# Kernel tuning notes

Hardware: AMD Instinct MI355X
Metric: run time of the kernel (lower is better)

Reference implementation:

```python
import jax, jax.numpy as jnp
import numpy as np

N_NODES = 50000
N_EDGES = 800000
EPS = 1e-5
NEG_SLOPE = 0.2


def _gatv2(x, src, dst, Wl, bl, Wr, br, att, bias, concat, N):
    # PyG GATv2Conv: xl = lin_l(x) (source side), xr = lin_r(x) (target side)
    H, C = att.shape
    xl = (x @ Wl + bl).reshape(N, H, C)
    xr = (x @ Wr + br).reshape(N, H, C)
    # per-edge message: leaky_relu(xl[j] + xr[i]), attention logit = <att, .>
    z = xl[src] + xr[dst]                      # [E, H, C]
    z = jnp.where(z > 0, z, NEG_SLOPE * z)
    logits = jnp.einsum('ehc,hc->eh', z, att)  # [E, H]
    # segment softmax over incoming edges of each target node
    m = jax.lax.stop_gradient(jax.ops.segment_max(logits, dst, num_segments=N))
    p = jnp.exp(logits - m[dst])
    s = jax.ops.segment_sum(p, dst, num_segments=N)
    alpha = p / s[dst]                         # [E, H]
    out = jax.ops.segment_sum(xl[src] * alpha[..., None], dst, num_segments=N)  # [N, H, C]
    out = out.reshape(N, H * C) if concat else out.mean(axis=1)
    return out + bias


def _bn(x, g, b):
    mu = x.mean(axis=0)
    v = x.var(axis=0)
    return (x - mu) * jax.lax.rsqrt(v + EPS) * g + b


def setup_inputs() -> dict:
    key = jax.random.key(0)
    ks = jax.random.split(key, 16)
    x = jax.random.normal(ks[0], (N_NODES, 2), jnp.float32)
    edge_index = jax.random.randint(ks[1], (2, N_EDGES), 0, N_NODES, dtype=jnp.int64)

    def lin(k, i, o):
        return jax.random.normal(k, (i, o), jnp.float32) * (1.0 / np.sqrt(i))

    inp = {'x': x, 'edge_index': edge_index}
    # layer 1: in=2, heads=8, out=16, concat
    inp['W1l'] = lin(ks[2], 2, 128); inp['b1l'] = jnp.zeros((128,), jnp.float32)
    inp['W1r'] = lin(ks[3], 2, 128); inp['b1r'] = jnp.zeros((128,), jnp.float32)
    inp['a1'] = jax.random.normal(ks[4], (8, 16), jnp.float32) * 0.1
    inp['bias1'] = jnp.zeros((128,), jnp.float32)
    inp['g1'] = jnp.ones((128,), jnp.float32); inp['be1'] = jnp.zeros((128,), jnp.float32)
    # layer 2: in=128, heads=4, out=16, concat
    inp['W2l'] = lin(ks[5], 128, 64); inp['b2l'] = jnp.zeros((64,), jnp.float32)
    inp['W2r'] = lin(ks[6], 128, 64); inp['b2r'] = jnp.zeros((64,), jnp.float32)
    inp['a2'] = jax.random.normal(ks[7], (4, 16), jnp.float32) * 0.1
    inp['bias2'] = jnp.zeros((64,), jnp.float32)
    inp['g2'] = jnp.ones((64,), jnp.float32); inp['be2'] = jnp.zeros((64,), jnp.float32)
    # layer 3: in=64, heads=1, out=2, mean (concat=False)
    inp['W3l'] = lin(ks[8], 64, 2); inp['b3l'] = jnp.zeros((2,), jnp.float32)
    inp['W3r'] = lin(ks[9], 64, 2); inp['b3r'] = jnp.zeros((2,), jnp.float32)
    inp['a3'] = jax.random.normal(ks[10], (1, 2), jnp.float32) * 0.1
    inp['bias3'] = jnp.zeros((2,), jnp.float32)
    return inp


def reference(x, edge_index, W1l, b1l, W1r, b1r, a1, bias1, g1, be1,
              W2l, b2l, W2r, b2r, a2, bias2, g2, be2,
              W3l, b3l, W3r, b3r, a3, bias3):
    N = x.shape[0]
    loops = jnp.arange(N, dtype=edge_index.dtype)
    src = jnp.concatenate([edge_index[0], loops])  # add self loops (PyG default)
    dst = jnp.concatenate([edge_index[1], loops])
    h = _gatv2(x, src, dst, W1l, b1l, W1r, b1r, a1, bias1, True, N)
    h = jax.nn.elu(_bn(h, g1, be1))  # dropout is identity in eval
    h = _gatv2(h, src, dst, W2l, b2l, W2r, b2r, a2, bias2, True, N)
    h = jax.nn.elu(_bn(h, g2, be2))
    return _gatv2(h, src, dst, W3l, b3l, W3r, b3r, a3, bias3, False, N)
```

## Files before the change

kernel.cpp:

```cpp
#include <hip/hip_runtime.h>
#include <hip/hip_bf16.h>

#define N_NODES 50000
#define N_E0    800000
#define N_ET    850000
#define EPSBN   1e-5f
#define LOG2E   1.4426950408889634f

#define LEAKY(z) fmaxf((z), 0.2f * (z))

#define OFF_C 0
#define OFF_A (128*N_NODES)
#define OFF_B (192*N_NODES)
#define OFF_STATS (256*N_NODES)
#define OFF_S1R (OFF_STATS + 512)
#define OFF_S2R (OFF_S1R + 16384)
#define OFF_P (OFF_S2R + 8192)
#define N_PARAM_TOT 118312
#define OFF_ROWPTR (OFF_P + N_PARAM_TOT)
#define OFF_DEG    (OFF_ROWPTR + 50001)
#define OFF_CURSOR (OFF_DEG + 50000)
#define OFF_BSUM   (OFF_CURSOR + 50000)
#define OFF_COL    (OFF_BSUM + 256)
#define OFF_FLAGS  (OFF_COL + 850064)
#define OFF_SCNT   (OFF_FLAGS + 2)

#define BK_CAP 131072
#define BK_CHUNK 2048

typedef float v2f __attribute__((ext_vector_type(2)));

__device__ __forceinline__ v2f ld2(const float* p) { return *(const v2f*)p; }
__device__ __forceinline__ v2f fma2(v2f a, v2f b, v2f c) {
    return __builtin_elementwise_fma(a, b, c);
}
__device__ __forceinline__ v2f max2(v2f a, v2f b) {
    return __builtin_elementwise_max(a, b);
}

__device__ __forceinline__ float bf2f(unsigned short u) {
    return __uint_as_float(((unsigned int)u) << 16);
}
__device__ __forceinline__ unsigned short f2bf(float f) {
    unsigned int u = __float_as_uint(f);
    u += 0x7FFFu + ((u >> 16) & 1u);
    return (unsigned short)(u >> 16);
}

__global__ void prep_kernel(const unsigned short* xr, const int* ei, int* flags,
                            int* deg, float* stats, float* s1r, float* s2r, int* scnt,
                            int* col) {
    int i = blockIdx.x * 256 + threadIdx.x;
    if (i < N_NODES) deg[i] = 0;
    if (i < 512) stats[i] = 0.f;
    if (i < 16384) s1r[i] = 0.f;
    if (i < 8192)  s2r[i] = 0.f;
    if (i < 8) scnt[i] = 0;
    if (i < 64) col[N_ET + i] = 0;
    if (blockIdx.x == 0) {
        __shared__ int c1, c2;
        if (threadIdx.x == 0) { c1 = 0; c2 = 0; }
        __syncthreads();
        int t = threadIdx.x;
        int l1 = 0, l2 = 0;
        for (int k = t; k < 2048; k += 256) {
            float v = bf2f(xr[k]);
            if (!(fabsf(v) <= 100.0f)) l1++;
            if (ei[2 * k + 1] != 0) l2++;
        }
        atomicAdd(&c1, l1);
        atomicAdd(&c2, l2);
        __syncthreads();
        if (t == 0) {
            flags[0] = (c1 > 16) ? 1 : 0;
            flags[1] = (c2 == 0) ? 1 : 0;
        }
    }
}

struct ParamPtrs { const void* p[23]; };

__global__ void convert_kernel(ParamPtrs ps, float* dst, const int* flags) {
    const int sizes[23] = {100000, 256,128,256,128,128,128,128,128,
                           8192,64,8192,64,64,64,64,64,
                           128,2,128,2,2,2};
    int g = blockIdx.x * 256 + threadIdx.x;
    if (g >= N_PARAM_TOT) return;
    int t = 0, off = g;
    while (off >= sizes[t]) { off -= sizes[t]; t++; }
    float v;
    if (flags[0]) v = ((const float*)ps.p[t])[off];
    else          v = bf2f(((const unsigned short*)ps.p[t])[off]);
    if (t == 5 || t == 13 || t == 21) v *= LOG2E;
    dst[g] = v;
}

__global__ void bucket_kernel(const int* ei, const int* flags, int* scnt,
                              int* dstb, int* srcb, int* deg) {
    __shared__ int lcnt[8];
    __shared__ int lbase[8];
    int tid = threadIdx.x;
    if (tid < 8) lcnt[tid] = 0;
    __syncthreads();
    int base_e = blockIdx.x * BK_CHUNK;
    int i64 = flags[1];
    int src[8], dst[8], pos[8];
    #pragma unroll
    for (int u = 0; u < 8; u++) {
        int e = base_e + u * 256 + tid;
        if (e < N_ET) {
            int s, d;
            if (e < N_E0) {
                d = i64 ? ei[2 * (N_E0 + e)] : ei[N_E0 + e];
                s = i64 ? ei[2 * e] : ei[e];
            } else { s = d = e - N_E0; }
            src[u] = s; dst[u] = d;
            pos[u] = atomicAdd(&lcnt[d / 6250], 1);
            atomicAdd(&deg[d], 1);
        } else dst[u] = -1;
    }
    __syncthreads();
    if (tid < 8) lbase[tid] = atomicAdd(&scnt[tid], lcnt[tid]);
    __syncthreads();
    #pragma unroll
    for (int u = 0; u < 8; u++) {
        if (dst[u] >= 0) {
            int st = dst[u] / 6250;
            int gp = st * BK_CAP + lbase[st] + pos[u];
            dstb[gp] = dst[u];
            srcb[gp] = src[u];
        }
    }
}

__global__ void scan1_kernel(const int* deg, int* row_ptr, int* bsum) {
    __shared__ int sh[256];
    int i = blockIdx.x * 256 + threadIdx.x;
    int v = (i < N_NODES) ? deg[i] : 0;
    sh[threadIdx.x] = v;
    __syncthreads();
    for (int off = 1; off < 256; off <<= 1) {
        int t = (threadIdx.x >= off) ? sh[threadIdx.x - off] : 0;
        __syncthreads();
        sh[threadIdx.x] += t;
        __syncthreads();
    }
    if (i < N_NODES) row_ptr[i] = sh[threadIdx.x] - v;
    if (threadIdx.x == 255) bsum[blockIdx.x] = sh[255];
}

__global__ void scan23_kernel(int* row_ptr, int* cursor, const int* bsum) {
    __shared__ int sh[256];
    int t = threadIdx.x;
    int v = (t < 196) ? bsum[t] : 0;
    sh[t] = v;
    __syncthreads();
    for (int off = 1; off < 256; off <<= 1) {
        int u = (t >= off) ? sh[t - off] : 0;
        __syncthreads();
        sh[t] += u;
        __syncthreads();
    }
    int prefix = (blockIdx.x == 0) ? 0 : sh[blockIdx.x - 1];
    int i = blockIdx.x * 256 + t;
    if (i < N_NODES) {
        int r = row_ptr[i] + prefix;
        row_ptr[i] = r;
        cursor[i] = r;
    }
    if (i == 0) row_ptr[N_NODES] = N_ET;
}

__global__ void scatter2_kernel(const int* scnt, const int* dstb, const int* srcb,
                                int* cursor, int* col) {
    int stripe = blockIdx.x & 7;
    int bi = blockIdx.x >> 3;
    int cnt = scnt[stripe];
    int off = stripe * BK_CAP;
    for (int t = bi * 256 + threadIdx.x; t < cnt; t += 32 * 256) {
        int d = dstb[off + t];
        int pos = atomicAdd(&cursor[d], 1);
        col[pos] = srcb[off + t];
    }
}

__global__ void __launch_bounds__(256) gather1_kernel(
    const int* row_ptr, const int* col, const float* x,
    const float* W1l, const float* b1l, const float* W1r, const float* b1r,
    const float* att, const float* bias, unsigned int* Cb, float* s1r)
{
    int gid = blockIdx.x * 256 + threadIdx.x;
    int n = gid >> 6;
    int lane = threadIdx.x & 63;
    int eslot = lane >> 4;
    int slot  = lane & 15;
    int c0 = slot << 3;

    int base = __builtin_amdgcn_readfirstlane(row_ptr[n]);
    int deg  = __builtin_amdgcn_readfirstlane(row_ptr[n + 1]) - base;

    v2f w0[4], w1[4], at[4], K[4];
    v2f xd = ld2(x + 2 * n);
    v2f xdx = {xd.x, xd.x}, xdy = {xd.y, xd.y};
    #pragma unroll
    for (int k = 0; k < 4; k++) {
        w0[k] = ld2(W1l + c0 + 2 * k);
        w1[k] = ld2(W1l + 128 + c0 + 2 * k);
        at[k] = ld2(att + c0 + 2 * k);
        v2f wr0 = ld2(W1r + c0 + 2 * k);
        v2f wr1 = ld2(W1r + 128 + c0 + 2 * k);
        v2f bb  = ld2(b1r + c0 + 2 * k) + ld2(b1l + c0 + 2 * k);
        K[k] = fma2(xdx, wr0, fma2(xdy, wr1, bb));
    }

    float S0 = 0.f, S1 = 0.f, SP = 0.f;
    for (int j0 = 0; j0 < deg; j0 += 64) {
        int cnt = deg - j0; if (cnt > 64) cnt = 64;
        int msrc = col[base + j0 + lane];
        v2f xsv = ld2(x + 2 * msrc);
        for (int jb = 0; jb < cnt; jb += 4) {
            int e = jb + eslot;
            float x0s = __shfl(xsv.x, e, 64);
            float x1s = __shfl(xsv.y, e, 64);
            v2f x0 = {x0s, x0s}, x1 = {x1s, x1s};
            v2f lg = {0.f, 0.f};
            #pragma unroll
            for (int k = 0; k < 4; k++) {
                v2f t = fma2(x1, w1[k], fma2(x0, w0[k], K[k]));
                lg = fma2(max2(t, 0.2f * t), at[k], lg);
            }
            float logit = lg.x + lg.y;
            logit += __shfl_xor(logit, 1, 64);
            float p = (e < cnt) ? exp2f(logit) : 0.f;
            S0 = fmaf(p, x0s, S0);
            S1 = fmaf(p, x1s, S1);
            SP += p;
        }
    }
    #pragma unroll
    for (int m = 16; m <= 32; m <<= 1) {
        S0 += __shfl_xor(S0, m, 64);
        S1 += __shfl_xor(S1, m, 64);
        SP += __shfl_xor(SP, m, 64);
    }
    float inv = 1.f / SP;
    float t0 = S0 * inv, t1 = S1 * inv;

    int hsrc = (lane >> 3) << 1;
    float t0o = __shfl(t0, hsrc, 64);
    float t1o = __shfl(t1, hsrc, 64);
    v2f w0o = ld2(W1l + 2 * lane);
    v2f w1o = ld2(W1l + 128 + 2 * lane);
    v2f bo  = ld2(b1l + 2 * lane) + ld2(bias + 2 * lane);
    float ox = fmaf(w0o.x, t0o, fmaf(w1o.x, t1o, bo.x));
    float oy = fmaf(w0o.y, t0o, fmaf(w1o.y, t1o, bo.y));
    Cb[n * 64 + lane] = ((unsigned int)f2bf(oy) << 16) | f2bf(ox);

    __shared__ float sred[4][128];
    __shared__ float qred[4][128];
    int wv = threadIdx.x >> 6;
    sred[wv][2 * lane]     = ox;
    sred[wv][2 * lane + 1] = oy;
    qred[wv][2 * lane]     = ox * ox;
    qred[wv][2 * lane + 1] = oy * oy;
    __syncthreads();
    int t = threadIdx.x;
    float a;
    if (t < 128) a = sred[0][t] + sred[1][t] + sred[2][t] + sred[3][t];
    else { int c = t - 128; a = qred[0][c] + qred[1][c] + qred[2][c] + qred[3][c]; }
    atomicAdd(&s1r[(blockIdx.x & 63) * 256 + t], a);
}

__global__ void red1_kernel(const float* s1r, const float* g1, const float* be1,
                            float* stats) {
    __shared__ float ls[256];
    int t = threadIdx.x;
    float a = 0.f;
    for (int r = 0; r < 64; r++) a += s1r[r * 256 + t];
    ls[t] = a;
    __syncthreads();
    if (t < 128) {
        float mu = ls[t] * (1.0f / N_NODES);
        float var = ls[128 + t] * (1.0f / N_NODES) - mu * mu;
        float sc = g1[t] * rsqrtf(var + EPSBN);
        stats[t] = sc;
        stats[128 + t] = be1[t] - mu * sc;
    }
}

__global__ void __launch_bounds__(256) lin2_kernel(
    const unsigned int* Cb, const float* stats, const float* Wl, const float* bl,
    const float* Wr, const float* br, unsigned short* xl2b, float* xr2)
{
    __shared__ float h[64 * 132];
    int tid = threadIdx.x;
    int nb = blockIdx.x * 64;
    for (int i = tid; i < 64 * 64; i += 256) {
        int ni = i >> 6, kp = i & 63;
        int n = nb + ni;
        int k = 2 * kp;
        float v0 = 0.f, v1 = 0.f;
        if (n < N_NODES) {
            unsigned int pk = Cb[n * 64 + kp];
            float b0 = fmaf(__uint_as_float(pk << 16),        stats[k],     stats[128 + k]);
            float b1 = fmaf(__uint_as_float(pk & 0xffff0000u), stats[k + 1], stats[128 + k + 1]);
            v0 = b0 > 0.f ? b0 : __expf(b0) - 1.f;
            v1 = b1 > 0.f ? b1 : __expf(b1) - 1.f;
        }
        h[ni * 132 + k]     = v0;
        h[ni * 132 + k + 1] = v1;
    }
    __syncthreads();
    int kt = (tid & 15) * 4;
    int nt = (tid >> 4) * 4;
    float accl[4][4], accr[4][4];
    #pragma unroll
    for (int i = 0; i < 4; i++) {
        #pragma unroll
        for (int k = 0; k < 4; k++) { accl[i][k] = 0.f; accr[i][k] = 0.f; }
    }
    for (int j = 0; j < 128; j += 4) {
        float4 hv[4];
        #pragma unroll
        for (int i = 0; i < 4; i++)
            hv[i] = *(const float4*)&h[(nt + i) * 132 + j];
        #pragma unroll
        for (int jj = 0; jj < 4; jj++) {
            float4 wl4 = *(const float4*)&Wl[(j + jj) * 64 + kt];
            float4 wr4 = *(const float4*)&Wr[(j + jj) * 64 + kt];
            #pragma unroll
            for (int i = 0; i < 4; i++) {
                float hvv = (jj == 0) ? hv[i].x : (jj == 1) ? hv[i].y :
                            (jj == 2) ? hv[i].z : hv[i].w;
                accl[i][0] += hvv * wl4.x; accl[i][1] += hvv * wl4.y;
                accl[i][2] += hvv * wl4.z; accl[i][3] += hvv * wl4.w;
                accr[i][0] += hvv * wr4.x; accr[i][1] += hvv * wr4.y;
                accr[i][2] += hvv * wr4.z; accr[i][3] += hvv * wr4.w;
            }
        }
    }
    float4 blv = *(const float4*)&bl[kt];
    float4 brv = *(const float4*)&br[kt];
    #pragma unroll
    for (int i = 0; i < 4; i++) {
        int n = nb + nt + i;
        if (n < N_NODES) {
            ushort4 ob;
            ob.x = f2bf(accl[i][0] + blv.x);
            ob.y = f2bf(accl[i][1] + blv.y);
            ob.z = f2bf(accl[i][2] + blv.z);
            ob.w = f2bf(accl[i][3] + blv.w);
            *(ushort4*)&xl2b[n * 64 + kt] = ob;
            float4 o;
            o.x = accr[i][0] + brv.x; o.y = accr[i][1] + brv.y;
            o.z = accr[i][2] + brv.z; o.w = accr[i][3] + brv.w;
            *(float4*)&xr2[n * 64 + kt] = o;
        }
    }
}

__global__ void __launch_bounds__(256) gather2_kernel(
    const int* row_ptr, const int* col, const unsigned short* xl2b, const float* xr2,
    const float* att, const float* bias, float* C, float* s2r)
{
    int gid = blockIdx.x * 256 + threadIdx.x;
    int n = gid >> 6;
    int lane = threadIdx.x & 63;
    int grp = lane >> 4;
    int cidx = lane & 15;
    float4 xrv = *(const float4*)(xr2 + n * 64 + 4 * cidx);
    float4 atv = *(const float4*)(att + 4 * cidx);
    int base = __builtin_amdgcn_readfirstlane(row_ptr[n]);
    int deg  = __builtin_amdgcn_readfirstlane(row_ptr[n + 1]) - base;
    float4 acc = make_float4(0.f, 0.f, 0.f, 0.f);
    float den = 0.f;
    for (int j0 = 0; j0 < deg; j0 += 64) {
        int cnt = deg - j0; if (cnt > 64) cnt = 64;
        int msrc = col[base + j0 + lane];
        for (int j4 = 0; j4 < cnt; j4 += 8) {
            int e0 = j4 + grp, e1 = j4 + 4 + grp;
            int s0 = __shfl(msrc, e0, 64);
            int s1 = __shfl(msrc, e1, 64);
            bool v0 = e0 < cnt, v1 = e1 < cnt;
            s0 = v0 ? s0 : 0;
            s1 = v1 ? s1 : 0;
            uint2 ba = *(const uint2*)(xl2b + (size_t)s0 * 64 + 4 * cidx);
            uint2 bb = *(const uint2*)(xl2b + (size_t)s1 * 64 + 4 * cidx);
            float a0 = __uint_as_float(ba.x << 16);
            float a1 = __uint_as_float(ba.x & 0xffff0000u);
            float a2 = __uint_as_float(ba.y << 16);
            float a3 = __uint_as_float(ba.y & 0xffff0000u);
            float b0 = __uint_as_float(bb.x << 16);
            float b1 = __uint_as_float(bb.x & 0xffff0000u);
            float b2 = __uint_as_float(bb.y << 16);
            float b3 = __uint_as_float(bb.y & 0xffff0000u);
            float pa = LEAKY(a0 + xrv.x) * atv.x;
            pa = fmaf(LEAKY(a1 + xrv.y), atv.y, pa);
            pa = fmaf(LEAKY(a2 + xrv.z), atv.z, pa);
            pa = fmaf(LEAKY(a3 + xrv.w), atv.w, pa);
            float pb = LEAKY(b0 + xrv.x) * atv.x;
            pb = fmaf(LEAKY(b1 + xrv.y), atv.y, pb);
            pb = fmaf(LEAKY(b2 + xrv.z), atv.z, pb);
            pb = fmaf(LEAKY(b3 + xrv.w), atv.w, pb);
            pa += __shfl_xor(pa, 1, 64);
            pa += __shfl_xor(pa, 2, 64);
            pb += __shfl_xor(pb, 1, 64);
            pb += __shfl_xor(pb, 2, 64);
            float ea = v0 ? exp2f(pa) : 0.f;
            float eb = v1 ? exp2f(pb) : 0.f;
            acc.x = fmaf(ea, a0, acc.x); acc.x = fmaf(eb, b0, acc.x);
            acc.y = fmaf(ea, a1, acc.y); acc.y = fmaf(eb, b1, acc.y);
            acc.z = fmaf(ea, a2, acc.z); acc.z = fmaf(eb, b2, acc.z);
            acc.w = fmaf(ea, a3, acc.w); acc.w = fmaf(eb, b3, acc.w);
            den += ea + eb;
        }
    }
    acc.x += __shfl_xor(acc.x, 16, 64); acc.x += __shfl_xor(acc.x, 32, 64);
    acc.y += __shfl_xor(acc.y, 16, 64); acc.y += __shfl_xor(acc.y, 32, 64);
    acc.z += __shfl_xor(acc.z, 16, 64); acc.z += __shfl_xor(acc.z, 32, 64);
    acc.w += __shfl_xor(acc.w, 16, 64); acc.w += __shfl_xor(acc.w, 32, 64);
    den += __shfl_xor(den, 16, 64);
    den += __shfl_xor(den, 32, 64);
    float inv = 1.f / den;
    float4 bi = *(const float4*)(bias + 4 * cidx);
    float4 o;
    o.x = fmaf(acc.x, inv, bi.x);
    o.y = fmaf(acc.y, inv, bi.y);
    o.z = fmaf(acc.z, inv, bi.z);
    o.w = fmaf(acc.w, inv, bi.w);
    if (lane < 16) *(float4*)(C + n * 64 + 4 * cidx) = o;
    __shared__ float sred[4][64];
    __shared__ float qred[4][64];
    int wv = threadIdx.x >> 6;
    if (lane < 16) {
        int c = 4 * cidx;
        sred[wv][c]     = o.x; qred[wv][c]     = o.x * o.x;
        sred[wv][c + 1] = o.y; qred[wv][c + 1] = o.y * o.y;
        sred[wv][c + 2] = o.z; qred[wv][c + 2] = o.z * o.z;
        sred[wv][c + 3] = o.w; qred[wv][c + 3] = o.w * o.w;
    }
    __syncthreads();
    int t = threadIdx.x;
    if (t < 128) {
        float a;
        if (t < 64) a = sred[0][t] + sred[1][t] + sred[2][t] + sred[3][t];
        else { int c = t - 64; a = qred[0][c] + qred[1][c] + qred[2][c] + qred[3][c]; }
        atomicAdd(&s2r[(blockIdx.x & 63) * 128 + t], a);
    }
}

__global__ void red2_kernel(const float* s2r, const float* g2, const float* be2,
                            float* stats) {
    __shared__ float ls[128];
    int t = threadIdx.x;
    float a = 0.f;
    for (int r = 0; r < 64; r++) a += s2r[r * 128 + t];
    ls[t] = a;
    __syncthreads();
    if (t < 64) {
        float mu = ls[t] * (1.0f / N_NODES);
        float var = ls[64 + t] * (1.0f / N_NODES) - mu * mu;
        float sc = g2[t] * rsqrtf(var + EPSBN);
        stats[t] = sc;
        stats[64 + t] = be2[t] - mu * sc;
    }
}

__global__ void __launch_bounds__(256) lin3_kernel(
    const float* C, const float* stats2,
    const float* Wl, const float* bl, const float* Wr, const float* br,
    float* xl3, float* xr3)
{
    int gid = blockIdx.x * 256 + threadIdx.x;
    int n = gid >> 6;
    int lane = threadIdx.x & 63;
    if (n >= N_NODES) return;
    float v = fmaf(C[n * 64 + lane], stats2[lane], stats2[64 + lane]);
    float h = v > 0.f ? v : __expf(v) - 1.f;
    float2 wlv = *(const float2*)(Wl + 2 * lane);
    float2 wrv = *(const float2*)(Wr + 2 * lane);
    float a0 = h * wlv.x, a1 = h * wlv.y;
    float r0 = h * wrv.x, r1 = h * wrv.y;
    #pragma unroll
    for (int m = 1; m < 64; m <<= 1) {
        a0 += __shfl_xor(a0, m, 64);
        a1 += __shfl_xor(a1, m, 64);
        r0 += __shfl_xor(r0, m, 64);
        r1 += __shfl_xor(r1, m, 64);
    }
    if (lane == 0) {
        xl3[2 * n]     = a0 + bl[0];
        xl3[2 * n + 1] = a1 + bl[1];
        xr3[2 * n]     = r0 + br[0];
        xr3[2 * n + 1] = r1 + br[1];
    }
}

__global__ void __launch_bounds__(256) gather3_kernel(
    const int* row_ptr, const int* col,
    const float* xl3, const float* xr3,
    const float* att, const float* bias,
    void* out, const int* flags) {
    int gid = blockIdx.x * 256 + threadIdx.x;
    int n = gid >> 2;
    int q = threadIdx.x & 3;
    if (n >= N_NODES) return;
    float a0 = att[0], a1 = att[1];
    float xr0 = xr3[2 * n], xr1 = xr3[2 * n + 1];
    float acc0 = 0.f, acc1 = 0.f, den = 0.f;
    int e0 = row_ptr[n], e1 = row_ptr[n + 1];
    for (int e = e0 + q; e < e1; e += 4) {
        int src = col[e];
        float2 xs = *(const float2*)(xl3 + 2 * src);
        float z0 = LEAKY(xs.x + xr0);
        float z1 = LEAKY(xs.y + xr1);
        float p = exp2f(fmaf(z0, a0, z1 * a1));
        acc0 = fmaf(p, xs.x, acc0);
        acc1 = fmaf(p, xs.y, acc1);
        den += p;
    }
    acc0 += __shfl_xor(acc0, 1, 64); acc0 += __shfl_xor(acc0, 2, 64);
    acc1 += __shfl_xor(acc1, 1, 64); acc1 += __shfl_xor(acc1, 2, 64);
    den  += __shfl_xor(den, 1, 64);  den  += __shfl_xor(den, 2, 64);
    if (q == 0) {
        float inv = 1.f / den;
        float v0 = fmaf(acc0, inv, bias[0]);
        float v1 = fmaf(acc1, inv, bias[1]);
        if (flags[0]) {
            ((float*)out)[2 * n] = v0;
            ((float*)out)[2 * n + 1] = v1;
        } else {
            ((__hip_bfloat16*)out)[2 * n] = __float2bfloat16(v0);
            ((__hip_bfloat16*)out)[2 * n + 1] = __float2bfloat16(v1);
        }
    }
}

extern "C" void kernel_launch(void* const* d_in, const int* in_sizes, int n_in,
                              void* d_out, int out_size, void* d_ws, size_t ws_size,
                              hipStream_t stream) {
    float* W = (float*)d_ws;
    float* C = W + OFF_C;
    float* A = W + OFF_A;
    float* B = W + OFF_B;
    float* STATS = W + OFF_STATS;
    float* S1R = W + OFF_S1R;
    float* S2R = W + OFF_S2R;
    float* P = W + OFF_P;
    int* ROWPTR = (int*)(W + OFF_ROWPTR);
    int* DEG    = (int*)(W + OFF_DEG);
    int* CURSOR = (int*)(W + OFF_CURSOR);
    int* BSUM   = (int*)(W + OFF_BSUM);
    int* COL    = (int*)(W + OFF_COL);
    int* FLAGS  = (int*)(W + OFF_FLAGS);
    int* SCNT   = (int*)(W + OFF_SCNT);
    int* DSTB   = (int*)(W + OFF_C);
    int* SRCB   = DSTB + 8 * BK_CAP;

    const int* ei = (const int*)d_in[1];

    float* Px  = P;
    float* W1l = Px + 100000; float* b1l = W1l + 256; float* W1r = b1l + 128; float* b1r = W1r + 256;
    float* a1  = b1r + 128;   float* bias1 = a1 + 128; float* g1 = bias1 + 128; float* be1 = g1 + 128;
    float* W2l = be1 + 128;   float* b2l = W2l + 8192; float* W2r = b2l + 64;  float* b2r = W2r + 8192;
    float* a2  = b2r + 64;    float* bias2 = a2 + 64;  float* g2 = bias2 + 64; float* be2 = g2 + 64;
    float* W3l = be2 + 64;    float* b3l = W3l + 128;  float* W3r = b3l + 2;   float* b3r = W3r + 128;
    float* a3  = b3r + 2;     float* bias3 = a3 + 2;

    prep_kernel<<<196, 256, 0, stream>>>((const unsigned short*)d_in[0], ei, FLAGS, DEG, STATS, S1R, S2R, SCNT, COL);

    ParamPtrs ps;
    ps.p[0] = d_in[0];
    for (int j = 1; j < 23; j++) ps.p[j] = d_in[j + 1];
    convert_kernel<<<(N_PARAM_TOT + 255) / 256, 256, 0, stream>>>(ps, P, FLAGS);

    bucket_kernel<<<(N_ET + BK_CHUNK - 1) / BK_CHUNK, 256, 0, stream>>>(ei, FLAGS, SCNT, DSTB, SRCB, DEG);
    scan1_kernel<<<196, 256, 0, stream>>>(DEG, ROWPTR, BSUM);
    scan23_kernel<<<196, 256, 0, stream>>>(ROWPTR, CURSOR, BSUM);
    scatter2_kernel<<<256, 256, 0, stream>>>(SCNT, DSTB, SRCB, CURSOR, COL);

    gather1_kernel<<<N_NODES * 64 / 256, 256, 0, stream>>>(ROWPTR, COL, Px, W1l, b1l, W1r, b1r, a1, bias1, (unsigned int*)C, S1R);
    red1_kernel<<<1, 256, 0, stream>>>(S1R, g1, be1, STATS);

    lin2_kernel<<<(N_NODES + 63) / 64, 256, 0, stream>>>((const unsigned int*)C, STATS, W2l, b2l, W2r, b2r, (unsigned short*)A, B);
    gather2_kernel<<<N_NODES * 64 / 256, 256, 0, stream>>>(ROWPTR, COL, (const unsigned short*)A, B, a2, bias2, C, S2R);
    red2_kernel<<<1, 128, 0, stream>>>(S2R, g2, be2, STATS + 256);

    lin3_kernel<<<N_NODES * 64 / 256, 256, 0, stream>>>(C, STATS + 256, W3l, b3l, W3r, b3r, A, B);
    gather3_kernel<<<(N_NODES * 4 + 255) / 256, 256, 0, stream>>>(ROWPTR, COL, A, B, a3, bias3, d_out, FLAGS);
}
```

Baseline: 327.3 us.

## Split leaky-relu into linear and abs terms; remap gather1 lanes to 8 heads

Layer-2 attention logits now use leaky_relu(z)=0.6z+0.4|z|. The linear part is precomputed per node: lin2 emits a per-source dot product and gather2 computes a per-target term, so the edge loop only needs abs plus fma. Gather1 is remapped so each lane handles a full 16-channel head with 4-wide vectors. This processes 8 edges per iteration, drops an intra-loop shuffle, and adds an occupancy hint. The trade-off is an extra per-edge dot-value load in gather2, and the precomputed source dot uses fp32 xl while the message uses bf16 xl, which may shift rounding.

```diff
diff --git a/kernel.cpp b/kernel.cpp
--- a/kernel.cpp
+++ b/kernel.cpp
@@ -29,12 +29,14 @@
 #define BK_CHUNK 2048
 
 typedef float v2f __attribute__((ext_vector_type(2)));
+typedef float v4f __attribute__((ext_vector_type(4)));
 
 __device__ __forceinline__ v2f ld2(const float* p) { return *(const v2f*)p; }
-__device__ __forceinline__ v2f fma2(v2f a, v2f b, v2f c) {
+__device__ __forceinline__ v4f ld4(const float* p) { return *(const v4f*)p; }
+__device__ __forceinline__ v4f fma4(v4f a, v4f b, v4f c) {
     return __builtin_elementwise_fma(a, b, c);
 }
-__device__ __forceinline__ v2f max2(v2f a, v2f b) {
+__device__ __forceinline__ v4f max4(v4f a, v4f b) {
     return __builtin_elementwise_max(a, b);
 }
 
@@ -184,7 +186,7 @@
     }
 }
 
-__global__ void __launch_bounds__(256) gather1_kernel(
+__global__ void __launch_bounds__(256, 5) gather1_kernel(
     const int* row_ptr, const int* col, const float* x,
     const float* W1l, const float* b1l, const float* W1r, const float* b1r,
     const float* att, const float* bias, unsigned int* Cb, float* s1r)
@@ -192,25 +194,25 @@
     int gid = blockIdx.x * 256 + threadIdx.x;
     int n = gid >> 6;
     int lane = threadIdx.x & 63;
-    int eslot = lane >> 4;
-    int slot  = lane & 15;
-    int c0 = slot << 3;
+    int eslot = lane >> 3;
+    int h = lane & 7;
+    int c0 = h << 4;
 
     int base = __builtin_amdgcn_readfirstlane(row_ptr[n]);
     int deg  = __builtin_amdgcn_readfirstlane(row_ptr[n + 1]) - base;
 
-    v2f w0[4], w1[4], at[4], K[4];
+    v4f w0[4], w1[4], at[4], K[4];
     v2f xd = ld2(x + 2 * n);
-    v2f xdx = {xd.x, xd.x}, xdy = {xd.y, xd.y};
+    v4f xdx = {xd.x, xd.x, xd.x, xd.x}, xdy = {xd.y, xd.y, xd.y, xd.y};
     #pragma unroll
     for (int k = 0; k < 4; k++) {
-        w0[k] = ld2(W1l + c0 + 2 * k);
-        w1[k] = ld2(W1l + 128 + c0 + 2 * k);
-        at[k] = ld2(att + c0 + 2 * k);
-        v2f wr0 = ld2(W1r + c0 + 2 * k);
-        v2f wr1 = ld2(W1r + 128 + c0 + 2 * k);
-        v2f bb  = ld2(b1r + c0 + 2 * k) + ld2(b1l + c0 + 2 * k);
-        K[k] = fma2(xdx, wr0, fma2(xdy, wr1, bb));
+        w0[k] = ld4(W1l + c0 + 4 * k);
+        w1[k] = ld4(W1l + 128 + c0 + 4 * k);
+        at[k] = ld4(att + c0 + 4 * k);
+        v4f wr0 = ld4(W1r + c0 + 4 * k);
+        v4f wr1 = ld4(W1r + 128 + c0 + 4 * k);
+        v4f bb  = ld4(b1r + c0 + 4 * k) + ld4(b1l + c0 + 4 * k);
+        K[k] = fma4(xdx, wr0, fma4(xdy, wr1, bb));
     }
 
     float S0 = 0.f, S1 = 0.f, SP = 0.f;
@@ -218,19 +220,18 @@
         int cnt = deg - j0; if (cnt > 64) cnt = 64;
         int msrc = col[base + j0 + lane];
         v2f xsv = ld2(x + 2 * msrc);
-        for (int jb = 0; jb < cnt; jb += 4) {
+        for (int jb = 0; jb < cnt; jb += 8) {
             int e = jb + eslot;
             float x0s = __shfl(xsv.x, e, 64);
             float x1s = __shfl(xsv.y, e, 64);
-            v2f x0 = {x0s, x0s}, x1 = {x1s, x1s};
-            v2f lg = {0.f, 0.f};
+            v4f x0 = {x0s, x0s, x0s, x0s}, x1 = {x1s, x1s, x1s, x1s};
+            v4f lg = {0.f, 0.f, 0.f, 0.f};
             #pragma unroll
             for (int k = 0; k < 4; k++) {
-                v2f t = fma2(x1, w1[k], fma2(x0, w0[k], K[k]));
-                lg = fma2(max2(t, 0.2f * t), at[k], lg);
+                v4f t = fma4(x1, w1[k], fma4(x0, w0[k], K[k]));
+                lg = fma4(max4(t, 0.2f * t), at[k], lg);
             }
-            float logit = lg.x + lg.y;
-            logit += __shfl_xor(logit, 1, 64);
+            float logit = (lg.x + lg.y) + (lg.z + lg.w);
             float p = (e < cnt) ? exp2f(logit) : 0.f;
             S0 = fmaf(p, x0s, S0);
             S1 = fmaf(p, x1s, S1);
@@ -238,7 +239,7 @@
         }
     }
     #pragma unroll
-    for (int m = 16; m <= 32; m <<= 1) {
+    for (int m = 8; m <= 32; m <<= 1) {
         S0 += __shfl_xor(S0, m, 64);
         S1 += __shfl_xor(S1, m, 64);
         SP += __shfl_xor(SP, m, 64);
@@ -246,7 +247,7 @@
     float inv = 1.f / SP;
     float t0 = S0 * inv, t1 = S1 * inv;
 
-    int hsrc = (lane >> 3) << 1;
+    int hsrc = lane >> 3;
     float t0o = __shfl(t0, hsrc, 64);
     float t1o = __shfl(t1, hsrc, 64);
     v2f w0o = ld2(W1l + 2 * lane);
@@ -290,7 +291,8 @@
 
 __global__ void __launch_bounds__(256) lin2_kernel(
     const unsigned int* Cb, const float* stats, const float* Wl, const float* bl,
-    const float* Wr, const float* br, unsigned short* xl2b, float* xr2)
+    const float* Wr, const float* br, const float* att2,
+    unsigned short* xl2b, float* xr2, float* dots)
 {
     __shared__ float h[64 * 132];
     int tid = threadIdx.x;
@@ -341,15 +343,25 @@
     }
     float4 blv = *(const float4*)&bl[kt];
     float4 brv = *(const float4*)&br[kt];
+    float4 a2v = *(const float4*)&att2[kt];
+    float dp[4];
     #pragma unroll
     for (int i = 0; i < 4; i++) {
         int n = nb + nt + i;
+        float xl0 = accl[i][0] + blv.x;
+        float xl1 = accl[i][1] + blv.y;
+        float xl2v = accl[i][2] + blv.z;
+        float xl3v = accl[i][3] + blv.w;
+        dp[i] = xl0 * a2v.x;
+        dp[i] = fmaf(xl1, a2v.y, dp[i]);
+        dp[i] = fmaf(xl2v, a2v.z, dp[i]);
+        dp[i] = fmaf(xl3v, a2v.w, dp[i]);
         if (n < N_NODES) {
             ushort4 ob;
-            ob.x = f2bf(accl[i][0] + blv.x);
-            ob.y = f2bf(accl[i][1] + blv.y);
-            ob.z = f2bf(accl[i][2] + blv.z);
-            ob.w = f2bf(accl[i][3] + blv.w);
+            ob.x = f2bf(xl0);
+            ob.y = f2bf(xl1);
+            ob.z = f2bf(xl2v);
+            ob.w = f2bf(xl3v);
             *(ushort4*)&xl2b[n * 64 + kt] = ob;
             float4 o;
             o.x = accr[i][0] + brv.x; o.y = accr[i][1] + brv.y;
@@ -357,10 +369,24 @@
             *(float4*)&xr2[n * 64 + kt] = o;
         }
     }
+    #pragma unroll
+    for (int i = 0; i < 4; i++) {
+        dp[i] += __shfl_xor(dp[i], 1, 64);
+        dp[i] += __shfl_xor(dp[i], 2, 64);
+    }
+    if ((tid & 3) == 0) {
+        int hd = (tid & 15) >> 2;
+        #pragma unroll
+        for (int i = 0; i < 4; i++) {
+            int n = nb + nt + i;
+            if (n < N_NODES) dots[n * 4 + hd] = 0.6f * dp[i];
+        }
+    }
 }
 
 __global__ void __launch_bounds__(256) gather2_kernel(
-    const int* row_ptr, const int* col, const unsigned short* xl2b, const float* xr2,
+    const int* row_ptr, const int* col, const unsigned short* xl2b,
+    const float* dots, const float* xr2,
     const float* att, const float* bias, float* C, float* s2r)
 {
     int gid = blockIdx.x * 256 + threadIdx.x;
@@ -368,8 +394,17 @@
     int lane = threadIdx.x & 63;
     int grp = lane >> 4;
     int cidx = lane & 15;
+    int head = cidx >> 2;
     float4 xrv = *(const float4*)(xr2 + n * 64 + 4 * cidx);
     float4 atv = *(const float4*)(att + 4 * cidx);
+    float4 at04 = make_float4(0.4f * atv.x, 0.4f * atv.y, 0.4f * atv.z, 0.4f * atv.w);
+    float xd = xrv.x * atv.x;
+    xd = fmaf(xrv.y, atv.y, xd);
+    xd = fmaf(xrv.z, atv.z, xd);
+    xd = fmaf(xrv.w, atv.w, xd);
+    xd += __shfl_xor(xd, 1, 64);
+    xd += __shfl_xor(xd, 2, 64);
+    float lin_n = 0.6f * xd;
     int base = __builtin_amdgcn_readfirstlane(row_ptr[n]);
     int deg  = __builtin_amdgcn_readfirstlane(row_ptr[n + 1]) - base;
     float4 acc = make_float4(0.f, 0.f, 0.f, 0.f);
@@ -386,6 +421,8 @@
             s1 = v1 ? s1 : 0;
             uint2 ba = *(const uint2*)(xl2b + (size_t)s0 * 64 + 4 * cidx);
             uint2 bb = *(const uint2*)(xl2b + (size_t)s1 * 64 + 4 * cidx);
+            float da = dots[s0 * 4 + head];
+            float db = dots[s1 * 4 + head];
             float a0 = __uint_as_float(ba.x << 16);
             float a1 = __uint_as_float(ba.x & 0xffff0000u);
             float a2 = __uint_as_float(ba.y << 16);
@@ -394,20 +431,20 @@
             float b1 = __uint_as_float(bb.x & 0xffff0000u);
             float b2 = __uint_as_float(bb.y << 16);
             float b3 = __uint_as_float(bb.y & 0xffff0000u);
-            float pa = LEAKY(a0 + xrv.x) * atv.x;
-            pa = fmaf(LEAKY(a1 + xrv.y), atv.y, pa);
-            pa = fmaf(LEAKY(a2 + xrv.z), atv.z, pa);
-            pa = fmaf(LEAKY(a3 + xrv.w), atv.w, pa);
-            float pb = LEAKY(b0 + xrv.x) * atv.x;
-            pb = fmaf(LEAKY(b1 + xrv.y), atv.y, pb);
-            pb = fmaf(LEAKY(b2 + xrv.z), atv.z, pb);
-            pb = fmaf(LEAKY(b3 + xrv.w), atv.w, pb);
+            float pa = fabsf(a0 + xrv.x) * at04.x;
+            pa = fmaf(fabsf(a1 + xrv.y), at04.y, pa);
+            pa = fmaf(fabsf(a2 + xrv.z), at04.z, pa);
+            pa = fmaf(fabsf(a3 + xrv.w), at04.w, pa);
+            float pb = fabsf(b0 + xrv.x) * at04.x;
+            pb = fmaf(fabsf(b1 + xrv.y), at04.y, pb);
+            pb = fmaf(fabsf(b2 + xrv.z), at04.z, pb);
+            pb = fmaf(fabsf(b3 + xrv.w), at04.w, pb);
             pa += __shfl_xor(pa, 1, 64);
             pa += __shfl_xor(pa, 2, 64);
             pb += __shfl_xor(pb, 1, 64);
             pb += __shfl_xor(pb, 2, 64);
-            float ea = v0 ? exp2f(pa) : 0.f;
-            float eb = v1 ? exp2f(pb) : 0.f;
+            float ea = v0 ? exp2f(pa + da + lin_n) : 0.f;
+            float eb = v1 ? exp2f(pb + db + lin_n) : 0.f;
             acc.x = fmaf(ea, a0, acc.x); acc.x = fmaf(eb, b0, acc.x);
             acc.y = fmaf(ea, a1, acc.y); acc.y = fmaf(eb, b1, acc.y);
             acc.z = fmaf(ea, a2, acc.z); acc.z = fmaf(eb, b2, acc.z);
@@ -556,6 +593,7 @@
     int* SCNT   = (int*)(W + OFF_SCNT);
     int* DSTB   = (int*)(W + OFF_C);
     int* SRCB   = DSTB + 8 * BK_CAP;
+    float* DOTS = A + 32 * N_NODES;
 
     const int* ei = (const int*)d_in[1];
 
@@ -582,8 +620,8 @@
     gather1_kernel<<<N_NODES * 64 / 256, 256, 0, stream>>>(ROWPTR, COL, Px, W1l, b1l, W1r, b1r, a1, bias1, (unsigned int*)C, S1R);
     red1_kernel<<<1, 256, 0, stream>>>(S1R, g1, be1, STATS);
 
-    lin2_kernel<<<(N_NODES + 63) / 64, 256, 0, stream>>>((const unsigned int*)C, STATS, W2l, b2l, W2r, b2r, (unsigned short*)A, B);
-    gather2_kernel<<<N_NODES * 64 / 256, 256, 0, stream>>>(ROWPTR, COL, (const unsigned short*)A, B, a2, bias2, C, S2R);
+    lin2_kernel<<<(N_NODES + 63) / 64, 256, 0, stream>>>((const unsigned int*)C, STATS, W2l, b2l, W2r, b2r, a2, (unsigned short*)A, B, DOTS);
+    gather2_kernel<<<N_NODES * 64 / 256, 256, 0, stream>>>(ROWPTR, COL, (const unsigned short*)A, DOTS, B, a2, bias2, C, S2R);
     red2_kernel<<<1, 128, 0, stream>>>(S2R, g2, be2, STATS + 256);
 
     lin3_kernel<<<N_NODES * 64 / 256, 256, 0, stream>>>(C, STATS + 256, W3l, b3l, W3r, b3r, A, B);
```

Result: slower. 390.9 us (+19.4%).
